# Performance work log

Measured on AMD Instinct MI355X. Metric: run time of the kernel, lower is better.

## Reference

```python
import jax, jax.numpy as jnp
import numpy as np
from functools import partial

NP = 1024      # particles
T = 128        # timesteps
CUR_MIN, CUR_MAX = -2.0, 4.0
E_CRIT = 29000.0
F_STD = 0.005
G_STD = 0.01
NU = 1.0 / (G_STD * np.sqrt(2.0 * np.pi))

# VoC battery open-circuit-voltage curve constants
V_L, V_0 = -1.59614486, 4.13646328
GAMMA, ALPHA, BETA = 0.63726463, 1.40174122, 2.54478965


def voc(soc):
    return (V_L + (V_0 - V_L) * jnp.exp(GAMMA * (soc - 1.0))
            + ALPHA * V_L * (soc - 1.0)
            + (1.0 - ALPHA) * V_L * (jnp.exp(-BETA) - jnp.exp(-BETA * jnp.sqrt(soc))))


def setup_inputs() -> dict:
    key = jax.random.key(0)
    ks = jax.random.split(key, 11)
    soc_init = jax.random.uniform(ks[0], (NP, 1), jnp.float32, 0.3, 1.0)
    current = jax.random.normal(ks[1], (1, T), jnp.float32) * 0.5 + 1.0
    voltage_measured = 3.7 + 0.1 * jax.random.normal(ks[2], (1, T), jnp.float32)
    W1 = jax.random.normal(ks[3], (2, 1024), jnp.float32) / np.sqrt(2.0)
    b1 = jnp.zeros((1024,), jnp.float32)
    W2 = jax.random.normal(ks[4], (1024, 512), jnp.float32) / np.sqrt(1024.0)
    b2 = jnp.zeros((512,), jnp.float32)
    W3 = jax.random.normal(ks[5], (512, 1), jnp.float32) / np.sqrt(512.0)
    b3 = jnp.zeros((1,), jnp.float32)
    noise = jax.random.normal(ks[6], (T, NP, 1), jnp.float32)  # unit-std process noise
    u = jax.random.uniform(ks[7], (T,), jnp.float32)           # systematic-resampling offsets
    return {"soc_init": soc_init, "current": current, "voltage_measured": voltage_measured,
            "W1": W1, "b1": b1, "W2": W2, "b2": b2, "W3": W3, "b3": b3,
            "noise": noise, "u": u}


def _forward(soc_init, current, voltage_measured, W1, b1, W2, b2, W3, b3, noise, u):
    n = soc_init.shape[0]

    def mlp(x):  # [n,2] -> [n,1]
        z = jax.nn.sigmoid(x @ W1 + b1)
        z = jax.nn.sigmoid(z @ W2 + b2)
        return z @ W3 + b3

    def scale_I(I):
        return (I - CUR_MIN) / (CUR_MAX - CUR_MIN)

    cur = current[0]                       # [T]
    vmeas = voltage_measured[0]            # [T]
    cur_prev = jnp.concatenate([cur[:1], cur[:-1]])  # first step reuses current[0,0]

    def step(soc, xs):
        c_prev, c_t, vm, eps, ut = xs
        # --- prediction with previous current ---
        I = jnp.broadcast_to(c_prev, soc.shape)
        Z = mlp(jnp.concatenate([soc, scale_I(I)], axis=1))
        V = voc(soc) - I * Z
        soc = soc - I * V / E_CRIT + eps * F_STD
        soc = jnp.clip(soc, 1e-10, 1.0)
        # --- measurement update with current at t ---
        I = jnp.broadcast_to(c_t, soc.shape)
        sI = scale_I(I)
        Z = mlp(jnp.concatenate([soc, sI], axis=1))
        V = voc(soc) - I * Z
        logW = np.log(NU) - 0.5 * ((V - vm) / G_STD) ** 2  # [n,1]
        w = jnp.exp(logW - jnp.max(logW))[:, 0]
        wn = w / jnp.sum(w)
        # systematic resampling (deterministic given offset ut)
        cdf = jnp.cumsum(wn)
        pos = (ut + jnp.arange(n, dtype=jnp.float32)) / n
        idx = jnp.clip(jnp.searchsorted(cdf, pos), 0, n - 1)
        soc = soc[idx]
        # --- post-resample evaluation ---
        Z = mlp(jnp.concatenate([soc, sI], axis=1))
        V = voc(soc) - I * Z
        mse = jnp.mean((V - vm) ** 2)
        return soc, (mse, V[:, 0], soc[:, 0])

    soc0 = soc_init.astype(jnp.float32)
    _, (mses, Vs, socs) = jax.lax.scan(step, soc0, (cur_prev, cur, vmeas, noise, u))
    loss = jnp.mean(mses)        # == sum_t mse_t / T
    voltage = Vs.T               # [n, T]
    soc_hist = socs.T            # [n, T]
    return loss, voltage, soc_hist


def reference(soc_init, current, voltage_measured, W1, b1, W2, b2, W3, b3, noise, u):
    return _forward(soc_init, current, voltage_measured, W1, b1, W2, b2, W3, b3, noise, u)
```

## Files before the change

### kernel.cpp

```cpp
#include <hip/hip_runtime.h>
#include <stdint.h>

typedef __attribute__((ext_vector_type(8))) short short8;
typedef __attribute__((ext_vector_type(4))) float floatx4;

#define DONE_MAGIC 0x600DF00Du


__device__ __forceinline__ float sigm(float x) { return 1.0f / (1.0f + expf(-x)); }

__device__ __forceinline__ float vocf(float s) {
  const float V_L = -1.59614486f, V_0 = 4.13646328f;
  const float GAM = 0.63726463f, ALP = 1.40174122f, BET = 2.54478965f;
  return V_L + (V_0 - V_L) * expf(GAM * (s - 1.0f)) + ALP * V_L * (s - 1.0f)
       + (1.0f - ALP) * V_L * (expf(-BET) - expf(-BET * sqrtf(s)));
}

__device__ __forceinline__ unsigned short f2bf(float f) {
  unsigned u = __float_as_uint(f);
  u += 0x7FFFu + ((u >> 16) & 1u);
  return (unsigned short)(u >> 16);
}
__device__ __forceinline__ float bf2f(unsigned short b) {
  return __uint_as_float(((unsigned)b) << 16);
}

__device__ __forceinline__ float interp_c(const float* ctab, float s) {
  float f = s * 31.0f;
  float jf = fminf(floorf(f), 30.0f);
  int j = (int)jf;
  float u = f - jf;
  const float4 c = *(const float4*)&ctab[j * 4];
  return fmaf(fmaf(fmaf(c.w, u, c.z), u, c.y), u, c.x);
}

__device__ __forceinline__ int send_bl(float c, float u) {
  float C = c * 1024.0f;
  float sf = floorf(C - u);
  sf += (u + (sf + 1.0f) <= C) ? 1.0f : 0.0f;
  sf -= (u + sf > C) ? 1.0f : 0.0f;
  return (int)sf;
}

__device__ __forceinline__ float fast_exp2(float x) {
  float r;
  asm("v_exp_f32 %0, %1" : "=v"(r) : "v"(x));
  return r;
}


template<int C, int RM>
__device__ __forceinline__ float dpp_add_f(float x) {
  return __int_as_float(__builtin_amdgcn_update_dpp(0, __float_as_int(x), C, RM, 0xF, false));
}
template<int C, int RM>
__device__ __forceinline__ float dpp_old_f(float x) {
  return __int_as_float(__builtin_amdgcn_update_dpp(__float_as_int(x), __float_as_int(x), C, RM, 0xF, false));
}
template<int C, int RM>
__device__ __forceinline__ int dpp_old_i(int x) {
  return __builtin_amdgcn_update_dpp(x, x, C, RM, 0xF, false);
}
__device__ __forceinline__ float dpp_wshr1_f0(float x) {
  return __int_as_float(__builtin_amdgcn_update_dpp(0, __float_as_int(x), 0x138, 0xF, 0xF, true));
}
__device__ __forceinline__ int dpp_wshr1_i(int x, int old) {
  return __builtin_amdgcn_update_dpp(old, x, 0x138, 0xF, 0xF, false);
}
__device__ __forceinline__ int dpp_wshl1_i(int x, int old) {
  return __builtin_amdgcn_update_dpp(old, x, 0x130, 0xF, 0xF, false);
}

__device__ __forceinline__ float wave_iscan_add(float x) {
  x += dpp_add_f<0x111, 0xF>(x);
  x += dpp_add_f<0x112, 0xF>(x);
  x += dpp_add_f<0x114, 0xF>(x);
  x += dpp_add_f<0x118, 0xF>(x);
  x += dpp_add_f<0x142, 0xA>(x);
  x += dpp_add_f<0x143, 0xC>(x);
  return x;
}
__device__ __forceinline__ float wave_max_bcast(float x) {
  x = fmaxf(x, dpp_old_f<0xB1,  0xF>(x));
  x = fmaxf(x, dpp_old_f<0x4E,  0xF>(x));
  x = fmaxf(x, dpp_old_f<0x141, 0xF>(x));
  x = fmaxf(x, dpp_old_f<0x140, 0xF>(x));
  x = fmaxf(x, dpp_old_f<0x142, 0xA>(x));
  x = fmaxf(x, dpp_old_f<0x143, 0xC>(x));
  return __int_as_float(__builtin_amdgcn_readlane(__float_as_int(x), 63));
}
__device__ __forceinline__ int wave_iscan_max(int x) {
  x = max(x, dpp_old_i<0x111, 0xF>(x));
  x = max(x, dpp_old_i<0x112, 0xF>(x));
  x = max(x, dpp_old_i<0x114, 0xF>(x));
  x = max(x, dpp_old_i<0x118, 0xF>(x));
  x = max(x, dpp_old_i<0x142, 0xA>(x));
  x = max(x, dpp_old_i<0x143, 0xC>(x));
  return x;
}

__device__ __forceinline__ float rdlane_f(float x, int lane) {
  return __int_as_float(__builtin_amdgcn_readlane(__float_as_int(x), lane));
}

__device__ __forceinline__ void bar_lds() {
  asm volatile("s_waitcnt lgkmcnt(0)" ::: "memory");
  __builtin_amdgcn_s_barrier();
  asm volatile("" ::: "memory");
}


__global__ void __launch_bounds__(256)
k1_swizzle(const float* __restrict__ W2g, short* __restrict__ w2hiG, short* __restrict__ w2loG)
{
  int bid = blockIdx.x, tid = threadIdx.x;
  int pg = bid & 15, ng = bid >> 4;
  int u = pg * 256 + tid;
  int kb = u >> 7, l = u & 63, nt = (u >> 6) & 1, kq = l >> 4;
  int col = ng * 32 + nt * 16 + (l & 15);
  short8 hi8, lo8;
  #pragma unroll
  for (int j = 0; j < 8; j++) {
    int k = kb * 32 + kq * 8 + j;
    float w = W2g[k * 512 + col];
    unsigned short h = f2bf(w);
    hi8[j] = (short)h;
    lo8[j] = (short)f2bf(w - bf2f(h));
  }
  size_t off = ((size_t)ng * 4096 + u) * 8;
  *(short8*)(w2hiG + off) = hi8;
  *(short8*)(w2loG + off) = lo8;
}


__global__ void __launch_bounds__(256)
k2_gemm(const float* __restrict__ curg, const float* __restrict__ W1g,
        const float* __restrict__ b1g, const float* __restrict__ b2g,
        const float* __restrict__ W3g, const short* __restrict__ w2hiG,
        const short* __restrict__ w2loG, float* __restrict__ part)
{
  const int tid = threadIdx.x, bid = blockIdx.x;
  const int nh = bid / 72;
  const int rt = bid - nh * 72;
  const int wv = tid >> 6, ln = tid & 63;
  const int kq = ln >> 4;
  const int c = ln & 15, q = ln >> 4;

  const int pt = rt * 4 + wv;
  unsigned r = pt * 16 + c;
  unsigned t = r / 36u;
  int i = (int)(r - t * 36u);
  float soc = (float)(i - 1) * (1.0f / 31.0f);
  float sI = (curg[t] + 2.0f) / 6.0f;

  floatx4 acc[4][2];
  #pragma unroll
  for (int g = 0; g < 4; g++) {
    acc[g][0] = (floatx4){0.f, 0.f, 0.f, 0.f};
    acc[g][1] = (floatx4){0.f, 0.f, 0.f, 0.f};
  }

  const size_t ngBase = (size_t)(nh * 4) * 32768;

  for (int kb = 0; kb < 32; kb++) {
    int k0 = kb * 32 + kq * 8;
    floatx4 wa0 = *(const floatx4*)(W1g + k0);
    floatx4 wa1 = *(const floatx4*)(W1g + k0 + 4);
    floatx4 wb0 = *(const floatx4*)(W1g + 1024 + k0);
    floatx4 wb1 = *(const floatx4*)(W1g + 1024 + k0 + 4);
    floatx4 bb0 = *(const floatx4*)(b1g + k0);
    floatx4 bb1 = *(const floatx4*)(b1g + k0 + 4);
    short8 ah, al;
    #pragma unroll
    for (int j = 0; j < 4; j++) {
      float x = soc * wa0[j] + sI * wb0[j] + bb0[j];
      float z = __builtin_amdgcn_rcpf(1.0f + __expf(-x));
      unsigned short h = f2bf(z);
      ah[j] = (short)h;
      al[j] = (short)f2bf(z - bf2f(h));
    }
    #pragma unroll
    for (int j = 0; j < 4; j++) {
      float x = soc * wa1[j] + sI * wb1[j] + bb1[j];
      float z = __builtin_amdgcn_rcpf(1.0f + __expf(-x));
      unsigned short h = f2bf(z);
      ah[4 + j] = (short)h;
      al[4 + j] = (short)f2bf(z - bf2f(h));
    }

    const short* hi = w2hiG + ngBase + (size_t)(kb * 2) * 512 + ln * 8;
    const short* lo = w2loG + ngBase + (size_t)(kb * 2) * 512 + ln * 8;
    #pragma unroll
    for (int g = 0; g < 4; g++) {
      const short* hg = hi + (size_t)g * 32768;
      const short* lg = lo + (size_t)g * 32768;
      short8 bh0 = *(const short8*)(hg);
      short8 bh1 = *(const short8*)(hg + 512);
      short8 bl0 = *(const short8*)(lg);
      short8 bl1 = *(const short8*)(lg + 512);
      acc[g][0] = __builtin_amdgcn_mfma_f32_16x16x32_bf16(ah, bh0, acc[g][0], 0, 0, 0);
      acc[g][1] = __builtin_amdgcn_mfma_f32_16x16x32_bf16(ah, bh1, acc[g][1], 0, 0, 0);
      acc[g][0] = __builtin_amdgcn_mfma_f32_16x16x32_bf16(ah, bl0, acc[g][0], 0, 0, 0);
      acc[g][1] = __builtin_amdgcn_mfma_f32_16x16x32_bf16(ah, bl1, acc[g][1], 0, 0, 0);
      acc[g][0] = __builtin_amdgcn_mfma_f32_16x16x32_bf16(al, bh0, acc[g][0], 0, 0, 0);
      acc[g][1] = __builtin_amdgcn_mfma_f32_16x16x32_bf16(al, bh1, acc[g][1], 0, 0, 0);
    }
  }

  #pragma unroll
  for (int g = 0; g < 4; g++) {
    int ng = nh * 4 + g;
    float b20 = b2g[ng * 32 + c],      b21 = b2g[ng * 32 + 16 + c];
    float w30 = W3g[ng * 32 + c],      w31 = W3g[ng * 32 + 16 + c];
    #pragma unroll
    for (int r2 = 0; r2 < 4; r2++) {
      float v = w30 * sigm(acc[g][0][r2] + b20) + w31 * sigm(acc[g][1][r2] + b21);
      v += __shfl_xor(v, 1);
      v += __shfl_xor(v, 2);
      v += __shfl_xor(v, 4);
      v += __shfl_xor(v, 8);
      if (c == 0) part[(size_t)(pt * 16 + q * 4 + r2) * 16 + ng] = v;
    }
  }
}


__device__ __forceinline__ int swzi(int j) { return ((j & 3) << 8) | (j >> 2); }

__global__ void __launch_bounds__(256)
pf_seq(const float* __restrict__ soc_init, const float* __restrict__ curg,
       const float* __restrict__ vmeasg, const float* __restrict__ noise_g,
       const float* __restrict__ u_g, const float* __restrict__ part,
       const float* __restrict__ b3g, float* __restrict__ ctabG,
       unsigned* __restrict__ doneG, float* __restrict__ vout,
       float* __restrict__ sout, float* __restrict__ outp,
       unsigned* __restrict__ flag)
{
  __shared__ float ctabS[15872];
  __shared__ float2 pvS[2][1024];
  __shared__ int   markS[1024] __attribute__((aligned(16)));
  __shared__ int   chunkS[4] __attribute__((aligned(16)));
  __shared__ float2 msS[4] __attribute__((aligned(16)));
  __shared__ float lossS[4];
  __shared__ float Vrow[36];

  const int bid = blockIdx.x;
  const int tid = threadIdx.x;

  {
    if (tid < 36) {
      const float* p = part + (size_t)(bid * 36 + tid) * 16;
      float s = 0.f;
      #pragma unroll
      for (int i = 0; i < 16; i++) s += p[i];
      float Z = s + b3g[0];
      float node = (float)(tid - 1) * (1.0f / 31.0f);
      float nodc = fmaxf(node, 1e-10f);
      Vrow[tid] = vocf(nodc) - curg[bid] * Z;
    }
    __syncthreads();
    if (tid < 31) {
      float n0 = Vrow[tid], n1 = Vrow[tid + 1], n2 = Vrow[tid + 2], n3 = Vrow[tid + 3];
      float c0 = n1;
      float c1 = (-2.0f * n0 - 3.0f * n1 + 6.0f * n2 - n3) * (1.0f / 6.0f);
      float c2 = (n0 - 2.0f * n1 + n2) * 0.5f;
      float c3 = (-n0 + 3.0f * (n1 - n2) + n3) * (1.0f / 6.0f);
      *(float4*)&ctabG[(bid * 31 + tid) * 4] = make_float4(c0, c1, c2, c3);
    }
    __threadfence();
    __syncthreads();
    if (tid == 0)
      __hip_atomic_store(&doneG[bid], DONE_MAGIC, __ATOMIC_RELEASE, __HIP_MEMORY_SCOPE_AGENT);
  }

  if (bid != 0) {
    while (__hip_atomic_load(flag, __ATOMIC_ACQUIRE, __HIP_MEMORY_SCOPE_AGENT) != DONE_MAGIC) {
      __builtin_amdgcn_s_sleep(32);
    }
    if (bid <= 32) {
      int sl = bid - 1;
      int arr = sl & 1, pg = sl >> 1;
      const float* src = arr ? sout : vout;
      float* dst = outp + 1 + arr * 131072;
      float* tile = ctabS;
      int p0g = pg * 64;
      #pragma unroll 4
      for (int s = 0; s < 32; s++) {
        int tt = s * 4 + (tid >> 6);
        int p = tid & 63;
        tile[tt * 65 + p] = src[tt * 1024 + p0g + p];
      }
      __syncthreads();
      #pragma unroll 4
      for (int s = 0; s < 32; s++) {
        int pl = s * 2 + (tid >> 7);
        int tt = tid & 127;
        dst[(p0g + pl) * 128 + tt] = tile[tt * 65 + pl];
      }
    }
    return;
  }

  if (tid < 128) {
    while (__hip_atomic_load(&doneG[tid], __ATOMIC_ACQUIRE, __HIP_MEMORY_SCOPE_AGENT) != DONE_MAGIC)
      __builtin_amdgcn_s_sleep(1);
  }
  __syncthreads();

  const int w = tid >> 6, l = tid & 63;
  const int p0 = tid * 4;

  #pragma unroll
  for (int k = 0; k < 16; k++) {
    int i = tid + 256 * k;
    if (i < 3968) *(float4*)&ctabS[i * 4] = *(const float4*)&ctabG[i * 4];
  }
  float curA = curg[l],   curB = curg[64 + l];
  float vmA  = vmeasg[l], vmB  = vmeasg[64 + l];
  float uA   = u_g[l],    uB   = u_g[64 + l];
  *(int4*)&markS[p0] = make_int4(-1, -1, -1, -1);
  if (tid < 4) chunkS[tid] = -1;

  float sp0, sp1, sp2, sp3;
  {
    float4 s4 = *(const float4*)(soc_init + p0);
    float4 n4 = *(const float4*)(noise_g + p0);
    bar_lds();
    float c0 = rdlane_f(curA, 0);
    float c02 = c0 * (1.0f / 29000.0f);
    float spv[4];
    #pragma unroll
    for (int r = 0; r < 4; r++) {
      float si = ((const float*)&s4)[r];
      float V0 = interp_c(ctabS, si);
      float spn = fmaf(((const float*)&n4)[r], 0.005f, fmaf(-c02, V0, si));
      spv[r] = __builtin_amdgcn_fmed3f(spn, 1e-10f, 1.0f);
    }
    sp0 = spv[0]; sp1 = spv[1]; sp2 = spv[2]; sp3 = spv[3];
  }

  float lossAcc = 0.0f;

  for (int t = 0; t < 128; t++) {
    const float* ctab = ctabS + t * 124;
    const int cb = t & 1;
    float cI, vm, ut;
    if (t < 64) { cI = rdlane_f(curA, t); vm = rdlane_f(vmA, t); ut = rdlane_f(uA, t); }
    else        { cI = rdlane_f(curB, t - 64); vm = rdlane_f(vmB, t - 64); ut = rdlane_f(uB, t - 64); }
    float cI2 = cI * (1.0f / 29000.0f);

    int tn = (t < 127) ? t + 1 : 127;
    float4 noi4 = *(const float4*)(noise_g + tn * 1024 + p0);

    float V10 = interp_c(ctab, sp0);
    float V11 = interp_c(ctab, sp1);
    float V12 = interp_c(ctab, sp2);
    float V13 = interp_c(ctab, sp3);
    pvS[cb][tid]       = make_float2(sp0, V10);
    pvS[cb][256 + tid] = make_float2(sp1, V11);
    pvS[cb][512 + tid] = make_float2(sp2, V12);
    pvS[cb][768 + tid] = make_float2(sp3, V13);
    float d0 = V10 - vm, d1 = V11 - vm, d2 = V12 - vm, d3 = V13 - vm;
    float lw0 = d0 * d0 * -7213.4755594f;
    float lw1 = d1 * d1 * -7213.4755594f;
    float lw2 = d2 * d2 * -7213.4755594f;
    float lw3 = d3 * d3 * -7213.4755594f;

    float lmax = fmaxf(fmaxf(lw0, lw1), fmaxf(lw2, lw3));
    float mw = wave_max_bcast(lmax);
    float pr0, pr1, pr2, pr3, acc;
    {
      float w0 = fast_exp2(lw0 - mw); acc = w0;    pr0 = acc;
      float w1 = fast_exp2(lw1 - mw); acc += w1;   pr1 = acc;
      float w2 = fast_exp2(lw2 - mw); acc += w2;   pr2 = acc;
      float w3 = fast_exp2(lw3 - mw); acc += w3;   pr3 = acc;
    }
    float isc = wave_iscan_add(acc);
    if (l == 63) msS[w] = make_float2(mw, isc);
    bar_lds();

    float4 ms01 = *(const float4*)&msS[0];
    float4 ms23 = *(const float4*)&msS[2];
    float m = fmaxf(fmaxf(ms01.x, ms01.z), fmaxf(ms23.x, ms23.z));
    float f0 = fast_exp2(ms01.x - m), f1 = fast_exp2(ms01.z - m);
    float f2 = fast_exp2(ms23.x - m), f3 = fast_exp2(ms23.z - m);
    float t0 = ms01.y * f0, t1 = ms01.w * f1, t2 = ms23.y * f2, t3 = ms23.w * f3;
    float total = (t0 + t1) + (t2 + t3);
    float woff = (w > 0 ? t0 : 0.0f) + (w > 1 ? t1 : 0.0f) + (w > 2 ? t2 : 0.0f);
    float fw = (w == 0) ? f0 : ((w == 1) ? f1 : ((w == 2) ? f2 : f3));
    float exclw = dpp_wshr1_f0(isc);
    float rS = 1.0f / total;

    int se0 = send_bl(fmaf(exclw + pr0, fw, woff) * rS, ut);
    int se1 = send_bl(fmaf(exclw + pr1, fw, woff) * rS, ut);
    int se2 = send_bl(fmaf(exclw + pr2, fw, woff) * rS, ut);
    int se3 = send_bl(fmaf(exclw + pr3, fw, woff) * rS, ut);

    int nxt = dpp_wshl1_i(se0, se3);
    int tbase = t << 10;
    if (tid == 0 && se0 >= 0) { markS[0] = tbase; atomicMax(&chunkS[0], tbase); }
    if (se1 > se0 && se0 < 1023) {
      int s = se0 + 1, tg = tbase | (p0 + 1);
      markS[swzi(s)] = tg; atomicMax(&chunkS[s >> 8], tg);
    }
    if (se2 > se1 && se1 < 1023) {
      int s = se1 + 1, tg = tbase | (p0 + 2);
      markS[swzi(s)] = tg; atomicMax(&chunkS[s >> 8], tg);
    }
    if (se3 > se2 && se2 < 1023) {
      int s = se2 + 1, tg = tbase | (p0 + 3);
      markS[swzi(s)] = tg; atomicMax(&chunkS[s >> 8], tg);
    }
    if (l != 63) {
      if (nxt > se3 && se3 < 1023) {
        int s = se3 + 1, tg = tbase | (p0 + 4);
        markS[swzi(s)] = tg; atomicMax(&chunkS[s >> 8], tg);
      }
    } else {
      if (se3 < 1023) {
        int s = se3 + 1;
        int tg = (tid == 255) ? (tbase | 1023) : (tbase | (p0 + 4));
        atomicMax(&markS[swzi(s)], tg); atomicMax(&chunkS[s >> 8], tg);
      }
    }
    bar_lds();

    int mk0 = markS[tid],       mk1 = markS[256 + tid];
    int mk2 = markS[512 + tid], mk3 = markS[768 + tid];
    int4 ch4 = *(const int4*)chunkS;
    int q0 = mk0;
    int q1 = max(q0, mk1);
    int q2 = max(q1, mk2);
    int q3 = max(q2, mk3);
    int iscI = wave_iscan_max(q3);
    int ex = dpp_wshr1_i(iscI, -1);
    if (w > 0) ex = max(ex, ch4.x);
    if (w > 1) ex = max(ex, ch4.y);
    if (w > 2) ex = max(ex, ch4.z);

    int o0 = max(ex, q0) & 1023, o1 = max(ex, q1) & 1023;
    int o2 = max(ex, q2) & 1023, o3 = max(ex, q3) & 1023;
    float2 g0 = pvS[cb][swzi(o0)];
    float2 g1 = pvS[cb][swzi(o1)];
    float2 g2 = pvS[cb][swzi(o2)];
    float2 g3 = pvS[cb][swzi(o3)];

    *(float4*)(vout + t * 1024 + p0) = make_float4(g0.y, g1.y, g2.y, g3.y);
    *(float4*)(sout + t * 1024 + p0) = make_float4(g0.x, g1.x, g2.x, g3.x);

    float e0 = g0.y - vm, e1 = g1.y - vm, e2 = g2.y - vm, e3 = g3.y - vm;
    lossAcc = fmaf(e0, e0, lossAcc);
    lossAcc = fmaf(e1, e1, lossAcc);
    lossAcc = fmaf(e2, e2, lossAcc);
    lossAcc = fmaf(e3, e3, lossAcc);
    const float* nz = (const float*)&noi4;
    sp0 = __builtin_amdgcn_fmed3f(fmaf(nz[0], 0.005f, fmaf(-cI2, g0.y, g0.x)), 1e-10f, 1.0f);
    sp1 = __builtin_amdgcn_fmed3f(fmaf(nz[1], 0.005f, fmaf(-cI2, g1.y, g1.x)), 1e-10f, 1.0f);
    sp2 = __builtin_amdgcn_fmed3f(fmaf(nz[2], 0.005f, fmaf(-cI2, g2.y, g2.x)), 1e-10f, 1.0f);
    sp3 = __builtin_amdgcn_fmed3f(fmaf(nz[3], 0.005f, fmaf(-cI2, g3.y, g3.x)), 1e-10f, 1.0f);
  }

  float ls = wave_iscan_add(lossAcc);
  if (l == 63) lossS[w] = ls;
  bar_lds();
  if (tid == 0) {
    outp[0] = (lossS[0] + lossS[1] + lossS[2] + lossS[3]) * (1.0f / 131072.0f);
    __hip_atomic_store(flag, DONE_MAGIC, __ATOMIC_RELEASE, __HIP_MEMORY_SCOPE_AGENT);
  }
}


extern "C" void kernel_launch(void* const* d_in, const int* in_sizes, int n_in,
                              void* d_out, int out_size, void* d_ws, size_t ws_size,
                              hipStream_t stream) {
  const float* soc_init = (const float*)d_in[0];
  const float* cur      = (const float*)d_in[1];
  const float* vmeas    = (const float*)d_in[2];
  const float* W1       = (const float*)d_in[3];
  const float* b1       = (const float*)d_in[4];
  const float* W2       = (const float*)d_in[5];
  const float* b2       = (const float*)d_in[6];
  const float* W3       = (const float*)d_in[7];
  const float* b3       = (const float*)d_in[8];
  const float* noise    = (const float*)d_in[9];
  const float* u        = (const float*)d_in[10];
  float* out = (float*)d_out;
  char* ws = (char*)d_ws;

  short* w2hi     = (short*)ws;
  short* w2lo     = (short*)(ws + (1 << 20));
  float* part     = (float*)(ws + (2 << 20));
  char*  p3       = ws + (2 << 20) + 4608 * 16 * 4;
  float* ctabG    = (float*)p3;
  unsigned* doneG = (unsigned*)(p3 + 3968 * 16);
  unsigned* flag  = (unsigned*)(p3 + 3968 * 16 + 512);
  float* vout     = (float*)(p3 + 3968 * 16 + 1024);
  float* sout     = (float*)(p3 + 3968 * 16 + 1024 + (512 << 10));

  k1_swizzle<<<256, 256, 0, stream>>>(W2, w2hi, w2lo);
  k2_gemm<<<288, 256, 0, stream>>>(cur, W1, b1, b2, W3, w2hi, w2lo, part);
  pf_seq<<<128, 256, 0, stream>>>(soc_init, cur, vmeas, noise, u, part, b3,
                                  ctabG, doneG, vout, sout, out, flag);
}
```

Before: 341.7 us.

## Fuse swizzle, GEMM and particle filter into one persistent kernel with flag sync

Merges the three kernels into a single 256-block launch. Per-block release/acquire flags replace kernel boundaries between the W2 swizzle, the MLP grid GEMM and the per-timestep spline-table build. The sequential particle-filter block no longer waits for all tables before it starts. It streams each timestep's coefficients into shared memory a few steps ahead while later tables are still being produced, which overlaps the GEMM tail with the sequential loop and removes two launch gaps. The cost is spin-waiting, which depends on all 256 blocks being co-resident, and extra fences.

```diff
diff --git a/kernel.cpp b/kernel.cpp
--- a/kernel.cpp
+++ b/kernel.cpp
@@ -109,132 +109,29 @@
   asm volatile("" ::: "memory");
 }
 
+__device__ __forceinline__ unsigned acq(const unsigned* p) {
+  return __hip_atomic_load(p, __ATOMIC_ACQUIRE, __HIP_MEMORY_SCOPE_AGENT);
+}
+__device__ __forceinline__ void rel(unsigned* p) {
+  __hip_atomic_store(p, DONE_MAGIC, __ATOMIC_RELEASE, __HIP_MEMORY_SCOPE_AGENT);
+}
+
+__device__ __forceinline__ int swzi(int j) { return ((j & 3) << 8) | (j >> 2); }
+
 
 __global__ void __launch_bounds__(256)
-k1_swizzle(const float* __restrict__ W2g, short* __restrict__ w2hiG, short* __restrict__ w2loG)
-{
-  int bid = blockIdx.x, tid = threadIdx.x;
-  int pg = bid & 15, ng = bid >> 4;
-  int u = pg * 256 + tid;
-  int kb = u >> 7, l = u & 63, nt = (u >> 6) & 1, kq = l >> 4;
-  int col = ng * 32 + nt * 16 + (l & 15);
-  short8 hi8, lo8;
-  #pragma unroll
-  for (int j = 0; j < 8; j++) {
-    int k = kb * 32 + kq * 8 + j;
-    float w = W2g[k * 512 + col];
-    unsigned short h = f2bf(w);
-    hi8[j] = (short)h;
-    lo8[j] = (short)f2bf(w - bf2f(h));
-  }
-  size_t off = ((size_t)ng * 4096 + u) * 8;
-  *(short8*)(w2hiG + off) = hi8;
-  *(short8*)(w2loG + off) = lo8;
-}
-
-
-__global__ void __launch_bounds__(256)
-k2_gemm(const float* __restrict__ curg, const float* __restrict__ W1g,
-        const float* __restrict__ b1g, const float* __restrict__ b2g,
-        const float* __restrict__ W3g, const short* __restrict__ w2hiG,
-        const short* __restrict__ w2loG, float* __restrict__ part)
-{
-  const int tid = threadIdx.x, bid = blockIdx.x;
-  const int nh = bid / 72;
-  const int rt = bid - nh * 72;
-  const int wv = tid >> 6, ln = tid & 63;
-  const int kq = ln >> 4;
-  const int c = ln & 15, q = ln >> 4;
-
-  const int pt = rt * 4 + wv;
-  unsigned r = pt * 16 + c;
-  unsigned t = r / 36u;
-  int i = (int)(r - t * 36u);
-  float soc = (float)(i - 1) * (1.0f / 31.0f);
-  float sI = (curg[t] + 2.0f) / 6.0f;
-
-  floatx4 acc[4][2];
-  #pragma unroll
-  for (int g = 0; g < 4; g++) {
-    acc[g][0] = (floatx4){0.f, 0.f, 0.f, 0.f};
-    acc[g][1] = (floatx4){0.f, 0.f, 0.f, 0.f};
-  }
-
-  const size_t ngBase = (size_t)(nh * 4) * 32768;
-
-  for (int kb = 0; kb < 32; kb++) {
-    int k0 = kb * 32 + kq * 8;
-    floatx4 wa0 = *(const floatx4*)(W1g + k0);
-    floatx4 wa1 = *(const floatx4*)(W1g + k0 + 4);
-    floatx4 wb0 = *(const floatx4*)(W1g + 1024 + k0);
-    floatx4 wb1 = *(const floatx4*)(W1g + 1024 + k0 + 4);
-    floatx4 bb0 = *(const floatx4*)(b1g + k0);
-    floatx4 bb1 = *(const floatx4*)(b1g + k0 + 4);
-    short8 ah, al;
-    #pragma unroll
-    for (int j = 0; j < 4; j++) {
-      float x = soc * wa0[j] + sI * wb0[j] + bb0[j];
-      float z = __builtin_amdgcn_rcpf(1.0f + __expf(-x));
-      unsigned short h = f2bf(z);
-      ah[j] = (short)h;
-      al[j] = (short)f2bf(z - bf2f(h));
-    }
-    #pragma unroll
-    for (int j = 0; j < 4; j++) {
-      float x = soc * wa1[j] + sI * wb1[j] + bb1[j];
-      float z = __builtin_amdgcn_rcpf(1.0f + __expf(-x));
-      unsigned short h = f2bf(z);
-      ah[4 + j] = (short)h;
-      al[4 + j] = (short)f2bf(z - bf2f(h));
-    }
-
-    const short* hi = w2hiG + ngBase + (size_t)(kb * 2) * 512 + ln * 8;
-    const short* lo = w2loG + ngBase + (size_t)(kb * 2) * 512 + ln * 8;
-    #pragma unroll
-    for (int g = 0; g < 4; g++) {
-      const short* hg = hi + (size_t)g * 32768;
-      const short* lg = lo + (size_t)g * 32768;
-      short8 bh0 = *(const short8*)(hg);
-      short8 bh1 = *(const short8*)(hg + 512);
-      short8 bl0 = *(const short8*)(lg);
-      short8 bl1 = *(const short8*)(lg + 512);
-      acc[g][0] = __builtin_amdgcn_mfma_f32_16x16x32_bf16(ah, bh0, acc[g][0], 0, 0, 0);
-      acc[g][1] = __builtin_amdgcn_mfma_f32_16x16x32_bf16(ah, bh1, acc[g][1], 0, 0, 0);
-      acc[g][0] = __builtin_amdgcn_mfma_f32_16x16x32_bf16(ah, bl0, acc[g][0], 0, 0, 0);
-      acc[g][1] = __builtin_amdgcn_mfma_f32_16x16x32_bf16(ah, bl1, acc[g][1], 0, 0, 0);
-      acc[g][0] = __builtin_amdgcn_mfma_f32_16x16x32_bf16(al, bh0, acc[g][0], 0, 0, 0);
-      acc[g][1] = __builtin_amdgcn_mfma_f32_16x16x32_bf16(al, bh1, acc[g][1], 0, 0, 0);
-    }
-  }
-
-  #pragma unroll
-  for (int g = 0; g < 4; g++) {
-    int ng = nh * 4 + g;
-    float b20 = b2g[ng * 32 + c],      b21 = b2g[ng * 32 + 16 + c];
-    float w30 = W3g[ng * 32 + c],      w31 = W3g[ng * 32 + 16 + c];
-    #pragma unroll
-    for (int r2 = 0; r2 < 4; r2++) {
-      float v = w30 * sigm(acc[g][0][r2] + b20) + w31 * sigm(acc[g][1][r2] + b21);
-      v += __shfl_xor(v, 1);
-      v += __shfl_xor(v, 2);
-      v += __shfl_xor(v, 4);
-      v += __shfl_xor(v, 8);
-      if (c == 0) part[(size_t)(pt * 16 + q * 4 + r2) * 16 + ng] = v;
-    }
-  }
-}
-
-
-__device__ __forceinline__ int swzi(int j) { return ((j & 3) << 8) | (j >> 2); }
-
-__global__ void __launch_bounds__(256)
-pf_seq(const float* __restrict__ soc_init, const float* __restrict__ curg,
+pf_all(const float* __restrict__ soc_init, const float* __restrict__ curg,
        const float* __restrict__ vmeasg, const float* __restrict__ noise_g,
-       const float* __restrict__ u_g, const float* __restrict__ part,
-       const float* __restrict__ b3g, float* __restrict__ ctabG,
-       unsigned* __restrict__ doneG, float* __restrict__ vout,
-       float* __restrict__ sout, float* __restrict__ outp,
-       unsigned* __restrict__ flag)
+       const float* __restrict__ u_g, const float* __restrict__ W2g,
+       const float* __restrict__ W1g, const float* __restrict__ b1g,
+       const float* __restrict__ b2g, const float* __restrict__ W3g,
+       const float* __restrict__ b3g,
+       short* __restrict__ w2hiG, short* __restrict__ w2loG,
+       float* __restrict__ part, float* __restrict__ ctabG,
+       unsigned* __restrict__ k1doneG, unsigned* __restrict__ k2doneG,
+       unsigned* __restrict__ doneG,
+       float* __restrict__ vout, float* __restrict__ sout,
+       float* __restrict__ outp, unsigned* __restrict__ flag)
 {
   __shared__ float ctabS[15872];
   __shared__ float2 pvS[2][1024];
@@ -248,15 +145,139 @@
   const int tid = threadIdx.x;
 
   {
+    int pg = bid & 15, ng = bid >> 4;
+    int u = pg * 256 + tid;
+    int kb = u >> 7, l = u & 63, nt = (u >> 6) & 1, kq = l >> 4;
+    int col = ng * 32 + nt * 16 + (l & 15);
+    short8 hi8, lo8;
+    #pragma unroll
+    for (int j = 0; j < 8; j++) {
+      int k = kb * 32 + kq * 8 + j;
+      float w = W2g[k * 512 + col];
+      unsigned short h = f2bf(w);
+      hi8[j] = (short)h;
+      lo8[j] = (short)f2bf(w - bf2f(h));
+    }
+    size_t off = ((size_t)ng * 4096 + u) * 8;
+    *(short8*)(w2hiG + off) = hi8;
+    *(short8*)(w2loG + off) = lo8;
+    __threadfence();
+    __syncthreads();
+    if (tid == 0) rel(&k1doneG[bid]);
+  }
+
+  auto k2_unit = [&](int u) {
+    const int nh = u / 72;
+    const int rt = u - nh * 72;
+    if (tid < 64) {
+      while (acq(&k1doneG[nh * 64 + tid]) != DONE_MAGIC) __builtin_amdgcn_s_sleep(1);
+    }
+    __syncthreads();
+
+    const int wv = tid >> 6, ln = tid & 63;
+    const int kq = ln >> 4;
+    const int c = ln & 15, q = ln >> 4;
+    const int pt = rt * 4 + wv;
+    unsigned r = pt * 16 + c;
+    unsigned t = r / 36u;
+    int i = (int)(r - t * 36u);
+    float soc = (float)(i - 1) * (1.0f / 31.0f);
+    float sI = (curg[t] + 2.0f) / 6.0f;
+
+    floatx4 acc[4][2];
+    #pragma unroll
+    for (int g = 0; g < 4; g++) {
+      acc[g][0] = (floatx4){0.f, 0.f, 0.f, 0.f};
+      acc[g][1] = (floatx4){0.f, 0.f, 0.f, 0.f};
+    }
+    const size_t ngBase = (size_t)(nh * 4) * 32768;
+
+    for (int kb = 0; kb < 32; kb++) {
+      int k0 = kb * 32 + kq * 8;
+      floatx4 wa0 = *(const floatx4*)(W1g + k0);
+      floatx4 wa1 = *(const floatx4*)(W1g + k0 + 4);
+      floatx4 wb0 = *(const floatx4*)(W1g + 1024 + k0);
+      floatx4 wb1 = *(const floatx4*)(W1g + 1024 + k0 + 4);
+      floatx4 bb0 = *(const floatx4*)(b1g + k0);
+      floatx4 bb1 = *(const floatx4*)(b1g + k0 + 4);
+      short8 ah, al;
+      #pragma unroll
+      for (int j = 0; j < 4; j++) {
+        float x = soc * wa0[j] + sI * wb0[j] + bb0[j];
+        float z = __builtin_amdgcn_rcpf(1.0f + __expf(-x));
+        unsigned short h = f2bf(z);
+        ah[j] = (short)h;
+        al[j] = (short)f2bf(z - bf2f(h));
+      }
+      #pragma unroll
+      for (int j = 0; j < 4; j++) {
+        float x = soc * wa1[j] + sI * wb1[j] + bb1[j];
+        float z = __builtin_amdgcn_rcpf(1.0f + __expf(-x));
+        unsigned short h = f2bf(z);
+        ah[4 + j] = (short)h;
+        al[4 + j] = (short)f2bf(z - bf2f(h));
+      }
+      const short* hi = w2hiG + ngBase + (size_t)(kb * 2) * 512 + ln * 8;
+      const short* lo = w2loG + ngBase + (size_t)(kb * 2) * 512 + ln * 8;
+      #pragma unroll
+      for (int g = 0; g < 4; g++) {
+        const short* hg = hi + (size_t)g * 32768;
+        const short* lg = lo + (size_t)g * 32768;
+        short8 bh0 = *(const short8*)(hg);
+        short8 bh1 = *(const short8*)(hg + 512);
+        short8 bl0 = *(const short8*)(lg);
+        short8 bl1 = *(const short8*)(lg + 512);
+        acc[g][0] = __builtin_amdgcn_mfma_f32_16x16x32_bf16(ah, bh0, acc[g][0], 0, 0, 0);
+        acc[g][1] = __builtin_amdgcn_mfma_f32_16x16x32_bf16(ah, bh1, acc[g][1], 0, 0, 0);
+        acc[g][0] = __builtin_amdgcn_mfma_f32_16x16x32_bf16(ah, bl0, acc[g][0], 0, 0, 0);
+        acc[g][1] = __builtin_amdgcn_mfma_f32_16x16x32_bf16(ah, bl1, acc[g][1], 0, 0, 0);
+        acc[g][0] = __builtin_amdgcn_mfma_f32_16x16x32_bf16(al, bh0, acc[g][0], 0, 0, 0);
+        acc[g][1] = __builtin_amdgcn_mfma_f32_16x16x32_bf16(al, bh1, acc[g][1], 0, 0, 0);
+      }
+    }
+
+    #pragma unroll
+    for (int g = 0; g < 4; g++) {
+      int ng = nh * 4 + g;
+      float b20 = b2g[ng * 32 + c], b21 = b2g[ng * 32 + 16 + c];
+      float w30 = W3g[ng * 32 + c], w31 = W3g[ng * 32 + 16 + c];
+      #pragma unroll
+      for (int r2 = 0; r2 < 4; r2++) {
+        float v = w30 * sigm(acc[g][0][r2] + b20) + w31 * sigm(acc[g][1][r2] + b21);
+        v += __shfl_xor(v, 1);
+        v += __shfl_xor(v, 2);
+        v += __shfl_xor(v, 4);
+        v += __shfl_xor(v, 8);
+        if (c == 0) part[(size_t)(pt * 16 + q * 4 + r2) * 16 + ng] = v;
+      }
+    }
+    __threadfence();
+    __syncthreads();
+    if (tid == 0) rel(&k2doneG[u]);
+  };
+
+  k2_unit(bid);
+  if (bid >= 128 && bid < 160) k2_unit(256 + (bid - 128));
+
+  if (bid < 128) {
+    const int t = bid;
+    const int rt0 = (36 * t) >> 6;
+    const int rt1 = (36 * t + 35) >> 6;
+    if (tid < 8) {
+      int rr = (tid < 4) ? rt0 : rt1;
+      int u = (tid & 3) * 72 + rr;
+      while (acq(&k2doneG[u]) != DONE_MAGIC) __builtin_amdgcn_s_sleep(1);
+    }
+    __syncthreads();
     if (tid < 36) {
-      const float* p = part + (size_t)(bid * 36 + tid) * 16;
+      const float* p = part + (size_t)(t * 36 + tid) * 16;
       float s = 0.f;
       #pragma unroll
       for (int i = 0; i < 16; i++) s += p[i];
       float Z = s + b3g[0];
       float node = (float)(tid - 1) * (1.0f / 31.0f);
       float nodc = fmaxf(node, 1e-10f);
-      Vrow[tid] = vocf(nodc) - curg[bid] * Z;
+      Vrow[tid] = vocf(nodc) - curg[t] * Z;
     }
     __syncthreads();
     if (tid < 31) {
@@ -265,19 +286,16 @@
       float c1 = (-2.0f * n0 - 3.0f * n1 + 6.0f * n2 - n3) * (1.0f / 6.0f);
       float c2 = (n0 - 2.0f * n1 + n2) * 0.5f;
       float c3 = (-n0 + 3.0f * (n1 - n2) + n3) * (1.0f / 6.0f);
-      *(float4*)&ctabG[(bid * 31 + tid) * 4] = make_float4(c0, c1, c2, c3);
+      *(float4*)&ctabG[(t * 31 + tid) * 4] = make_float4(c0, c1, c2, c3);
     }
     __threadfence();
     __syncthreads();
-    if (tid == 0)
-      __hip_atomic_store(&doneG[bid], DONE_MAGIC, __ATOMIC_RELEASE, __HIP_MEMORY_SCOPE_AGENT);
+    if (tid == 0) rel(&doneG[t]);
   }
 
   if (bid != 0) {
-    while (__hip_atomic_load(flag, __ATOMIC_ACQUIRE, __HIP_MEMORY_SCOPE_AGENT) != DONE_MAGIC) {
-      __builtin_amdgcn_s_sleep(32);
-    }
     if (bid <= 32) {
+      while (acq(flag) != DONE_MAGIC) __builtin_amdgcn_s_sleep(32);
       int sl = bid - 1;
       int arr = sl & 1, pg = sl >> 1;
       const float* src = arr ? sout : vout;
@@ -301,20 +319,26 @@
     return;
   }
 
-  if (tid < 128) {
-    while (__hip_atomic_load(&doneG[tid], __ATOMIC_ACQUIRE, __HIP_MEMORY_SCOPE_AGENT) != DONE_MAGIC)
-      __builtin_amdgcn_s_sleep(1);
-  }
-  __syncthreads();
-
   const int w = tid >> 6, l = tid & 63;
   const int p0 = tid * 4;
 
-  #pragma unroll
-  for (int k = 0; k < 16; k++) {
-    int i = tid + 256 * k;
-    if (i < 3968) *(float4*)&ctabS[i * 4] = *(const float4*)&ctabG[i * 4];
-  }
+  float4 stA = {0.f, 0.f, 0.f, 0.f}, stB = {0.f, 0.f, 0.f, 0.f};
+  unsigned pollReg = DONE_MAGIC;
+  if (tid < 4) {
+    while (acq(&doneG[tid]) != DONE_MAGIC) __builtin_amdgcn_s_sleep(1);
+  }
+  __syncthreads();
+  if (tid < 31) {
+    #pragma unroll
+    for (int j = 0; j < 4; j++)
+      *(float4*)&ctabS[j * 124 + tid * 4] = *(const float4*)&ctabG[(j * 31 + tid) * 4];
+    while (acq(&doneG[4]) != DONE_MAGIC) __builtin_amdgcn_s_sleep(1);
+    stA = *(const float4*)&ctabG[(4 * 31 + tid) * 4];
+    while (acq(&doneG[5]) != DONE_MAGIC) __builtin_amdgcn_s_sleep(1);
+    stB = *(const float4*)&ctabG[(5 * 31 + tid) * 4];
+    pollReg = __hip_atomic_load(&doneG[6], __ATOMIC_RELAXED, __HIP_MEMORY_SCOPE_AGENT);
+  }
+
   float curA = curg[l],   curB = curg[64 + l];
   float vmA  = vmeasg[l], vmB  = vmeasg[64 + l];
   float uA   = u_g[l],    uB   = u_g[64 + l];
@@ -342,6 +366,25 @@
   float lossAcc = 0.0f;
 
   for (int t = 0; t < 128; t++) {
+    if (tid < 31) {
+      int twr = t + 4;
+      if (twr < 128) {
+        float4 wv4 = (t & 1) ? stB : stA;
+        *(float4*)&ctabS[twr * 124 + tid * 4] = wv4;
+      }
+      int tld = t + 6;
+      if (tld < 128) {
+        if (pollReg != DONE_MAGIC) {
+          while (acq(&doneG[tld]) != DONE_MAGIC) __builtin_amdgcn_s_sleep(1);
+        }
+        float4 v = *(const float4*)&ctabG[(tld * 31 + tid) * 4];
+        if (t & 1) stB = v; else stA = v;
+        pollReg = (tld + 1 < 128)
+          ? __hip_atomic_load(&doneG[tld + 1], __ATOMIC_RELAXED, __HIP_MEMORY_SCOPE_AGENT)
+          : DONE_MAGIC;
+      }
+    }
+
     const float* ctab = ctabS + t * 124;
     const int cb = t & 1;
     float cI, vm, ut;
@@ -463,9 +506,12 @@
   float ls = wave_iscan_add(lossAcc);
   if (l == 63) lossS[w] = ls;
   bar_lds();
+  asm volatile("s_waitcnt vmcnt(0)" ::: "memory");
+  __threadfence();
+  __syncthreads();
   if (tid == 0) {
     outp[0] = (lossS[0] + lossS[1] + lossS[2] + lossS[3]) * (1.0f / 131072.0f);
-    __hip_atomic_store(flag, DONE_MAGIC, __ATOMIC_RELEASE, __HIP_MEMORY_SCOPE_AGENT);
+    rel(flag);
   }
 }
 
@@ -487,18 +533,21 @@
   float* out = (float*)d_out;
   char* ws = (char*)d_ws;
 
-  short* w2hi     = (short*)ws;
-  short* w2lo     = (short*)(ws + (1 << 20));
-  float* part     = (float*)(ws + (2 << 20));
-  char*  p3       = ws + (2 << 20) + 4608 * 16 * 4;
-  float* ctabG    = (float*)p3;
-  unsigned* doneG = (unsigned*)(p3 + 3968 * 16);
-  unsigned* flag  = (unsigned*)(p3 + 3968 * 16 + 512);
-  float* vout     = (float*)(p3 + 3968 * 16 + 1024);
-  float* sout     = (float*)(p3 + 3968 * 16 + 1024 + (512 << 10));
-
-  k1_swizzle<<<256, 256, 0, stream>>>(W2, w2hi, w2lo);
-  k2_gemm<<<288, 256, 0, stream>>>(cur, W1, b1, b2, W3, w2hi, w2lo, part);
-  pf_seq<<<128, 256, 0, stream>>>(soc_init, cur, vmeas, noise, u, part, b3,
-                                  ctabG, doneG, vout, sout, out, flag);
-}
+  short* w2hi       = (short*)ws;
+  short* w2lo       = (short*)(ws + (1 << 20));
+  float* part       = (float*)(ws + (2 << 20));
+  char*  p3         = ws + (2 << 20) + 4608 * 16 * 4;
+  float* ctabG      = (float*)p3;
+  unsigned* doneG   = (unsigned*)(p3 + 63488);
+  unsigned* k1doneG = (unsigned*)(p3 + 64000);
+  unsigned* k2doneG = (unsigned*)(p3 + 65024);
+  unsigned* flag    = (unsigned*)(p3 + 66304);
+  float* vout       = (float*)(p3 + 66560);
+  float* sout       = vout + 131072;
+
+  pf_all<<<256, 256, 0, stream>>>(soc_init, cur, vmeas, noise, u,
+                                  W2, W1, b1, b2, W3, b3,
+                                  w2hi, w2lo, part, ctabG,
+                                  k1doneG, k2doneG, doneG,
+                                  vout, sout, out, flag);
+}
```

Measured after the change: 426.0 us. 24.7% more time.
